# Kernel tuning notes

Measured on AMD Instinct MI355X. Metric: run time of the kernel, lower is better.

The kernel has to match this reference:

```python
import jax, jax.numpy as jnp
import numpy as np

N, C = 262144, 512
EPS = 1e-7


def setup_inputs() -> dict:
    key = jax.random.key(0)
    k1, k2, k3 = jax.random.split(key, 3)
    close_er = jax.random.normal(k1, (N, C), dtype=jnp.float32)
    y = jax.random.randint(k2, (N,), 0, C, dtype=jnp.int64)
    max_dis = jax.random.normal(k3, (C,), dtype=jnp.float32)
    margin = jnp.float32(0.5)
    return {"close_er": close_er, "y": y, "max_dis": max_dis, "margin": margin}


def reference(close_er, y, max_dis, margin):
    # Original: for each class i, take samples with y==i, compute
    # -log(clamp(sigmoid(close_er[idx, i] - max_dis[i] - margin))).mean(),
    # then average over classes that have at least one sample.
    num_classes = max_dis.shape[0]
    # Per-sample gather of its own-class distance: close_er[n, y[n]]
    ce = jnp.take_along_axis(close_er, y[:, None], axis=1)[:, 0]  # [N]
    md = max_dis[y]  # [N]
    gap = jax.nn.sigmoid(ce - md - margin)
    gap = jnp.clip(gap, EPS, 1.0 - EPS)
    nll = -jnp.log(gap)  # [N]
    # Per-class sum and count in one segment-reduce pass over N.
    sums = jax.ops.segment_sum(nll, y, num_segments=num_classes)  # [C]
    counts = jax.ops.segment_sum(jnp.ones_like(nll), y, num_segments=num_classes)  # [C]
    nonempty = counts > 0
    means = jnp.where(nonempty, sums / jnp.maximum(counts, 1.0), 0.0)
    j = jnp.sum(nonempty).astype(means.dtype)
    return jnp.sum(means) / j
```

## Files before the change

kernel.cpp:

```cpp
#include <hip/hip_runtime.h>

#define N_CLASSES 512
#define EPS_F 1e-7f
#define BLOCK 1024


__global__ __launch_bounds__(BLOCK) void nll_part_kernel(
    const float* __restrict__ close_er,
    const int*   __restrict__ y,
    const float* __restrict__ max_dis,
    const float* __restrict__ margin_p,
    float*          __restrict__ p_sums,
    unsigned short* __restrict__ p_cnts,
    int n)
{
    __shared__ float        s_md[N_CLASSES];
    __shared__ float        s_sum[N_CLASSES];
    __shared__ unsigned int s_cnt[N_CLASSES];

    const int tid = threadIdx.x;
    const float margin = margin_p[0];

    if (tid < N_CLASSES) {
        s_md[tid]  = max_dis[tid];
        s_sum[tid] = 0.0f;
        s_cnt[tid] = 0u;
    }
    __syncthreads();

    const int i = blockIdx.x * BLOCK + tid;
    if (i < n) {
        const int c = y[i];
        const float ce = close_er[(size_t)i * N_CLASSES + c];
        const float x  = ce - s_md[c] - margin;
        float s = 1.0f / (1.0f + __expf(-x));
        s = fminf(fmaxf(s, EPS_F), 1.0f - EPS_F);
        atomicAdd(&s_sum[c], -__logf(s));
        atomicAdd(&s_cnt[c], 1u);
    }
    __syncthreads();

    if (tid < N_CLASSES) {
        const size_t o = (size_t)blockIdx.x * N_CLASSES + tid;
        p_sums[o] = s_sum[tid];
        p_cnts[o] = (unsigned short)s_cnt[tid];
    }
}

__global__ __launch_bounds__(1024) void finalize_part_kernel(
    const float*          __restrict__ p_sums,
    const unsigned short* __restrict__ p_cnts,
    float* __restrict__ out,
    int R)
{
    __shared__ float        s1[1024];
    __shared__ unsigned int c1[1024];
    __shared__ float        s_red[32];

    const int t  = threadIdx.x;
    const int c  = t & (N_CLASSES - 1);
    const int b0 = t >> 9;

    float        sum = 0.0f;
    unsigned int cnt = 0u;
    #pragma unroll 4
    for (int b = b0; b < R; b += 2) {
        sum += p_sums[(size_t)b * N_CLASSES + c];
        cnt += p_cnts[(size_t)b * N_CLASSES + c];
    }
    s1[t] = sum;
    c1[t] = cnt;
    __syncthreads();

    float m = 0.0f, j = 0.0f;
    if (t < N_CLASSES) {
        const float        S = s1[t] + s1[t + 512];
        const unsigned int C = c1[t] + c1[t + 512];
        if (C > 0u) { m = S / (float)C; j = 1.0f; }
    }
    for (int off = 32; off > 0; off >>= 1) {
        m += __shfl_down(m, off);
        j += __shfl_down(j, off);
    }
    if ((t & 63) == 0) {
        s_red[(t >> 6) * 2]     = m;
        s_red[(t >> 6) * 2 + 1] = j;
    }
    __syncthreads();
    if (t == 0) {
        float M = 0.0f, J = 0.0f;
        for (int w = 0; w < 16; ++w) {
            M += s_red[w * 2];
            J += s_red[w * 2 + 1];
        }
        out[0] = M / J;
    }
}


__global__ __launch_bounds__(BLOCK) void nll_hist_kernel(
    const float* __restrict__ close_er,
    const int*   __restrict__ y,
    const float* __restrict__ max_dis,
    const float* __restrict__ margin_p,
    float* __restrict__ g_sums,
    float* __restrict__ g_counts,
    int n)
{
    __shared__ float        s_md[N_CLASSES];
    __shared__ float        s_sum[N_CLASSES];
    __shared__ unsigned int s_cnt[N_CLASSES];

    const int tid = threadIdx.x;
    const float margin = margin_p[0];

    if (tid < N_CLASSES) {
        s_md[tid]  = max_dis[tid];
        s_sum[tid] = 0.0f;
        s_cnt[tid] = 0u;
    }
    __syncthreads();

    const int i = blockIdx.x * BLOCK + tid;
    if (i < n) {
        const int c = y[i];
        const float ce = close_er[(size_t)i * N_CLASSES + c];
        const float x  = ce - s_md[c] - margin;
        float s = 1.0f / (1.0f + __expf(-x));
        s = fminf(fmaxf(s, EPS_F), 1.0f - EPS_F);
        atomicAdd(&s_sum[c], -__logf(s));
        atomicAdd(&s_cnt[c], 1u);
    }
    __syncthreads();

    if (tid < N_CLASSES) {
        const unsigned int cnt = s_cnt[tid];
        if (cnt != 0u) {
            atomicAdd(&g_sums[tid],   s_sum[tid]);
            atomicAdd(&g_counts[tid], (float)cnt);
        }
    }
}

__global__ __launch_bounds__(512) void finalize_kernel(
    const float* __restrict__ g_sums,
    const float* __restrict__ g_counts,
    float* __restrict__ out)
{
    __shared__ float s_red[16];
    const int t = threadIdx.x;
    float m = 0.0f, j = 0.0f;
    const float cnt = g_counts[t];
    if (cnt > 0.0f) { m = g_sums[t] / cnt; j = 1.0f; }
    for (int off = 32; off > 0; off >>= 1) {
        m += __shfl_down(m, off);
        j += __shfl_down(j, off);
    }
    if ((t & 63) == 0) {
        s_red[(t >> 6) * 2]     = m;
        s_red[(t >> 6) * 2 + 1] = j;
    }
    __syncthreads();
    if (t == 0) {
        float M = 0.0f, J = 0.0f;
        for (int w = 0; w < 8; ++w) {
            M += s_red[w * 2];
            J += s_red[w * 2 + 1];
        }
        out[0] = M / J;
    }
}


extern "C" void kernel_launch(void* const* d_in, const int* in_sizes, int n_in,
                              void* d_out, int out_size, void* d_ws, size_t ws_size,
                              hipStream_t stream) {
    const float* close_er = (const float*)d_in[0];
    const int*   y        = (const int*)d_in[1];
    const float* max_dis  = (const float*)d_in[2];
    const float* margin   = (const float*)d_in[3];
    float* out = (float*)d_out;

    const int n    = in_sizes[1];
    const int grid = (n + BLOCK - 1) / BLOCK;

    const size_t needA = (size_t)grid * N_CLASSES * (sizeof(float) + sizeof(unsigned short));

    if (ws_size >= needA) {
        float*          p_sums = (float*)d_ws;
        unsigned short* p_cnts = (unsigned short*)(p_sums + (size_t)grid * N_CLASSES);
        nll_part_kernel<<<grid, BLOCK, 0, stream>>>(close_er, y, max_dis, margin,
                                                    p_sums, p_cnts, n);
        finalize_part_kernel<<<1, 1024, 0, stream>>>(p_sums, p_cnts, out, grid);
    } else {
        float* g_sums   = (float*)d_ws;
        float* g_counts = g_sums + N_CLASSES;
        hipMemsetAsync(d_ws, 0, 2 * N_CLASSES * sizeof(float), stream);
        nll_hist_kernel<<<grid, BLOCK, 0, stream>>>(close_er, y, max_dis, margin,
                                                    g_sums, g_counts, n);
        finalize_kernel<<<1, N_CLASSES, 0, stream>>>(g_sums, g_counts, out);
    }
}
```

Baseline: 22.74 us.

## Split partial-sum reduction into a parallel two-stage reduce and use nontemporal gather loads

The per-block partial histograms (256 rows × 512 classes) were previously reduced by a single 1024-thread block, which serialises roughly 1.5 MB of reads on one CU. A new reduce kernel spreads this over 16 blocks, each summing 16 rows, and the final single-block kernel then reads only 16 rows. The scattered single-element gathers from close_er now use nontemporal loads to avoid polluting the cache. The cost is one extra kernel launch and a small intermediate buffer, and the workspace must be slightly larger to take this path.

```diff
diff --git a/kernel.cpp b/kernel.cpp
--- a/kernel.cpp
+++ b/kernel.cpp
@@ -3,6 +3,7 @@
 #define N_CLASSES 512
 #define EPS_F 1e-7f
 #define BLOCK 1024
+#define RB 16
 
 
 __global__ __launch_bounds__(BLOCK) void nll_part_kernel(
@@ -31,7 +32,7 @@
     const int i = blockIdx.x * BLOCK + tid;
     if (i < n) {
         const int c = y[i];
-        const float ce = close_er[(size_t)i * N_CLASSES + c];
+        const float ce = __builtin_nontemporal_load(&close_er[(size_t)i * N_CLASSES + c]);
         const float x  = ce - s_md[c] - margin;
         float s = 1.0f / (1.0f + __expf(-x));
         s = fminf(fmaxf(s, EPS_F), 1.0f - EPS_F);
@@ -47,26 +48,60 @@
     }
 }
 
-__global__ __launch_bounds__(1024) void finalize_part_kernel(
+__global__ __launch_bounds__(1024) void reduce_part_kernel(
     const float*          __restrict__ p_sums,
     const unsigned short* __restrict__ p_cnts,
-    float* __restrict__ out,
+    float* __restrict__ q_sums,
+    float* __restrict__ q_cnts,
     int R)
 {
-    __shared__ float        s1[1024];
-    __shared__ unsigned int c1[1024];
-    __shared__ float        s_red[32];
-
-    const int t  = threadIdx.x;
-    const int c  = t & (N_CLASSES - 1);
-    const int b0 = t >> 9;
+    __shared__ float s1[1024];
+    __shared__ float c1[1024];
+
+    const int t = threadIdx.x;
+    const int c = t & (N_CLASSES - 1);
+    const int g = t >> 9;
+    const int r0 = blockIdx.x * RB;
 
     float        sum = 0.0f;
     unsigned int cnt = 0u;
-    #pragma unroll 4
-    for (int b = b0; b < R; b += 2) {
-        sum += p_sums[(size_t)b * N_CLASSES + c];
-        cnt += p_cnts[(size_t)b * N_CLASSES + c];
+    #pragma unroll
+    for (int k = g; k < RB; k += 2) {
+        const int r = r0 + k;
+        if (r < R) {
+            sum += p_sums[(size_t)r * N_CLASSES + c];
+            cnt += p_cnts[(size_t)r * N_CLASSES + c];
+        }
+    }
+    s1[t] = sum;
+    c1[t] = (float)cnt;
+    __syncthreads();
+
+    if (t < N_CLASSES) {
+        const size_t o = (size_t)blockIdx.x * N_CLASSES + t;
+        q_sums[o] = s1[t] + s1[t + 512];
+        q_cnts[o] = c1[t] + c1[t + 512];
+    }
+}
+
+__global__ __launch_bounds__(1024) void finalize_part_kernel(
+    const float* __restrict__ q_sums,
+    const float* __restrict__ q_cnts,
+    float* __restrict__ out,
+    int nb)
+{
+    __shared__ float s1[1024];
+    __shared__ float c1[1024];
+    __shared__ float s_red[32];
+
+    const int t = threadIdx.x;
+    const int c = t & (N_CLASSES - 1);
+    const int g = t >> 9;
+
+    float sum = 0.0f, cnt = 0.0f;
+    for (int r = g; r < nb; r += 2) {
+        sum += q_sums[(size_t)r * N_CLASSES + c];
+        cnt += q_cnts[(size_t)r * N_CLASSES + c];
     }
     s1[t] = sum;
     c1[t] = cnt;
@@ -74,9 +109,9 @@
 
     float m = 0.0f, j = 0.0f;
     if (t < N_CLASSES) {
-        const float        S = s1[t] + s1[t + 512];
-        const unsigned int C = c1[t] + c1[t + 512];
-        if (C > 0u) { m = S / (float)C; j = 1.0f; }
+        const float S = s1[t] + s1[t + 512];
+        const float C = c1[t] + c1[t + 512];
+        if (C > 0.0f) { m = S / C; j = 1.0f; }
     }
     for (int off = 32; off > 0; off >>= 1) {
         m += __shfl_down(m, off);
@@ -124,7 +159,7 @@
     const int i = blockIdx.x * BLOCK + tid;
     if (i < n) {
         const int c = y[i];
-        const float ce = close_er[(size_t)i * N_CLASSES + c];
+        const float ce = __builtin_nontemporal_load(&close_er[(size_t)i * N_CLASSES + c]);
         const float x  = ce - s_md[c] - margin;
         float s = 1.0f / (1.0f + __expf(-x));
         s = fminf(fmaxf(s, EPS_F), 1.0f - EPS_F);
@@ -182,22 +217,28 @@
     float* out = (float*)d_out;
 
     const int n    = in_sizes[1];
-    const int grid = (n + BLOCK - 1) / BLOCK;
-
-    const size_t needA = (size_t)grid * N_CLASSES * (sizeof(float) + sizeof(unsigned short));
-
-    if (ws_size >= needA) {
+    const int R    = (n + BLOCK - 1) / BLOCK;
+    const int nb   = (R + RB - 1) / RB;
+
+    const size_t pA_bytes = (size_t)R * N_CLASSES * (sizeof(float) + sizeof(unsigned short));
+    const size_t qA_bytes = (size_t)nb * N_CLASSES * 2 * sizeof(float);
+
+    if (ws_size >= pA_bytes + qA_bytes) {
         float*          p_sums = (float*)d_ws;
-        unsigned short* p_cnts = (unsigned short*)(p_sums + (size_t)grid * N_CLASSES);
-        nll_part_kernel<<<grid, BLOCK, 0, stream>>>(close_er, y, max_dis, margin,
-                                                    p_sums, p_cnts, n);
-        finalize_part_kernel<<<1, 1024, 0, stream>>>(p_sums, p_cnts, out, grid);
+        unsigned short* p_cnts = (unsigned short*)(p_sums + (size_t)R * N_CLASSES);
+        float*          q_sums = (float*)((char*)d_ws + (size_t)R * N_CLASSES * 6);
+        float*          q_cnts = q_sums + (size_t)nb * N_CLASSES;
+
+        nll_part_kernel<<<R, BLOCK, 0, stream>>>(close_er, y, max_dis, margin,
+                                                 p_sums, p_cnts, n);
+        reduce_part_kernel<<<nb, 1024, 0, stream>>>(p_sums, p_cnts, q_sums, q_cnts, R);
+        finalize_part_kernel<<<1, 1024, 0, stream>>>(q_sums, q_cnts, out, nb);
     } else {
         float* g_sums   = (float*)d_ws;
         float* g_counts = g_sums + N_CLASSES;
         hipMemsetAsync(d_ws, 0, 2 * N_CLASSES * sizeof(float), stream);
-        nll_hist_kernel<<<grid, BLOCK, 0, stream>>>(close_er, y, max_dis, margin,
-                                                    g_sums, g_counts, n);
+        nll_hist_kernel<<<R, BLOCK, 0, stream>>>(close_er, y, max_dis, margin,
+                                                 g_sums, g_counts, n);
         finalize_kernel<<<1, N_CLASSES, 0, stream>>>(g_sums, g_counts, out);
     }
 }
```

New measurement: 19.20 us, median of 2. 1.18x faster.
